# Optimization experiments

Hardware: AMD Instinct MI355X
Metric: run time of the kernel (lower is better)

Reference implementation:

```python
import jax, jax.numpy as jnp
import numpy as np

B, INPUT_DIM, EMB_DIM = 16384, 2048, 768
DOMAIN_NUM, MEMORY_NUM, TAU = 9, 10, 32.0


def setup_inputs() -> dict:
    key = jax.random.key(0)
    k1, k2, k3, k4, k5 = jax.random.split(key, 5)
    feature = jax.random.normal(k1, (B, INPUT_DIM), dtype=jnp.float32)
    category = jax.random.randint(k2, (B,), 0, DOMAIN_NUM, dtype=jnp.int64)
    # Linear(input_dim, emb_dim, bias=False) weights: [emb_dim, input_dim]
    W_topic = jax.random.normal(k3, (EMB_DIM, INPUT_DIM), dtype=jnp.float32) * 0.02
    W_domain = jax.random.normal(k4, (EMB_DIM, INPUT_DIM), dtype=jnp.float32) * 0.02
    # domain_num Embedding(memory_num, emb_dim) tables, stacked: [D, M, E]
    memory_tables = jax.random.normal(k5, (DOMAIN_NUM, MEMORY_NUM, EMB_DIM), dtype=jnp.float32)
    return {"feature": feature, "W_topic": W_topic, "W_domain": W_domain,
            "memory_tables": memory_tables, "category": category}


def reference(feature, W_topic, W_domain, memory_tables, category):
    eps = 1e-12
    # F.normalize(feature, p=2, dim=-1)
    norm = jnp.maximum(jnp.linalg.norm(feature, axis=-1, keepdims=True), eps)
    feat = feature / norm                                   # [B, I]
    # per-sample gather of each sample's category memory table: [B, M, E]
    mem = memory_tables[category]
    # faithful quirk: loop over domain_num indexes the BATCH dim of the stack
    D = memory_tables.shape[0]
    mems_d = mem[:D]                                        # [D, M, E]
    t = feat @ W_topic.T                                    # [B, E]
    topic_att = jax.nn.softmax(jnp.einsum('be,dme->bdm', t, mems_d) * TAU, axis=-1)
    sep = jnp.einsum('bdm,dme->bde', topic_att, mems_d)     # [B, D, E]
    dproj = feat @ W_domain.T                               # [B, E]
    domain_att = jax.nn.softmax(jnp.einsum('bde,be->bd', sep, dproj) * TAU, axis=-1)
    return domain_att[:, None, :]                           # [B, 1, D]
```

## Files before the change

kernel.cpp:

```cpp
#include <hip/hip_runtime.h>
#include <math.h>

#define TAU_F 32.0f

typedef __attribute__((ext_vector_type(8))) _Float16 half8;
typedef __attribute__((ext_vector_type(2))) __fp16 half2v;
typedef __attribute__((ext_vector_type(4))) float f32x4;

union HU { uint4 u; half8 v; };

__device__ __forceinline__ void sync_lds_only() {
    asm volatile("s_waitcnt lgkmcnt(0)" ::: "memory");
    __builtin_amdgcn_s_barrier();
}

__global__ __launch_bounds__(256) void gproj2(
    const float* __restrict__ Wt, const float* __restrict__ Wd,
    const float* __restrict__ mem, const int* __restrict__ cat,
    float* __restrict__ P)
{
    __shared__ float Ml[96 * 36];
    __shared__ float Wl[32 * 68];

    const int bid = blockIdx.x;
    const int mat = bid >> 7;
    const int ks  = (bid >> 5) & 3;
    const int ct  = bid & 31;
    const int c0  = ct * 64;
    const int tid = threadIdx.x;
    const float* __restrict__ W = mat ? Wd : Wt;

    const int tr = tid >> 4;
    const int tc = tid & 15;

    float acc[6][4];
    #pragma unroll
    for (int j = 0; j < 6; ++j)
        #pragma unroll
        for (int q = 0; q < 4; ++q) acc[j][q] = 0.f;

    for (int ch = 0; ch < 6; ++ch) {
        __syncthreads();
        #pragma unroll
        for (int p = 0; p < 3; ++p) {
            const int idx = tid + 256 * p;
            const int r   = idx >> 3;
            const int kq  = idx & 7;
            float4 v = make_float4(0.f, 0.f, 0.f, 0.f);
            if (r < 90) {
                const int d = r / 10;
                const int mrow = cat[d] * 10 + (r - d * 10);
                v = *(const float4*)(mem + (size_t)mrow * 768 + ks * 192 + ch * 32 + kq * 4);
            }
            *(float4*)(Ml + r * 36 + kq * 4) = v;
        }
        #pragma unroll
        for (int p = 0; p < 2; ++p) {
            const int idx = tid + 256 * p;
            const int e   = idx >> 4;
            const int c4  = (idx & 15) * 4;
            *(float4*)(Wl + e * 68 + c4) =
                *(const float4*)(W + (size_t)(ks * 192 + ch * 32 + e) * 2048 + c0 + c4);
        }
        __syncthreads();

        #pragma unroll
        for (int e = 0; e < 32; e += 4) {
            float4 m4[6], w4[4];
            #pragma unroll
            for (int j = 0; j < 6; ++j) m4[j] = *(const float4*)(Ml + (tr * 6 + j) * 36 + e);
            #pragma unroll
            for (int q = 0; q < 4; ++q) w4[q] = *(const float4*)(Wl + (e + q) * 68 + tc * 4);
            #pragma unroll
            for (int j = 0; j < 6; ++j) {
                const float mv[4] = {m4[j].x, m4[j].y, m4[j].z, m4[j].w};
                #pragma unroll
                for (int q = 0; q < 4; ++q) {
                    acc[j][0] = fmaf(mv[q], w4[q].x, acc[j][0]);
                    acc[j][1] = fmaf(mv[q], w4[q].y, acc[j][1]);
                    acc[j][2] = fmaf(mv[q], w4[q].z, acc[j][2]);
                    acc[j][3] = fmaf(mv[q], w4[q].w, acc[j][3]);
                }
            }
        }
    }

    #pragma unroll
    for (int j = 0; j < 6; ++j) {
        float4 v = make_float4(acc[j][0], acc[j][1], acc[j][2], acc[j][3]);
        *(float4*)(P + (size_t)ks * 393216 + (size_t)(mat * 96 + tr * 6 + j) * 2048 + c0 + tc * 4) = v;
    }
}

__global__ __launch_bounds__(256) void split_g3(
    const float* __restrict__ P, unsigned short* __restrict__ gB)
{
    const int u  = blockIdx.x * 256 + threadIdx.x;
    const int n  = u >> 8;
    const int k0 = (u & 255) * 8;

    float s[8] = {0.f, 0.f, 0.f, 0.f, 0.f, 0.f, 0.f, 0.f};
    #pragma unroll
    for (int ks = 0; ks < 4; ++ks) {
        const float4 a = *(const float4*)(P + (size_t)ks * 393216 + (size_t)n * 2048 + k0);
        const float4 b = *(const float4*)(P + (size_t)ks * 393216 + (size_t)n * 2048 + k0 + 4);
        s[0] += a.x; s[1] += a.y; s[2] += a.z; s[3] += a.w;
        s[4] += b.x; s[5] += b.y; s[6] += b.z; s[7] += b.w;
    }
    union { _Float16 h[8]; uint4 u4; } hi, lo;
    #pragma unroll
    for (int e = 0; e < 8; ++e) {
        const _Float16 h = (_Float16)s[e];
        hi.h[e] = h;
        lo.h[e] = (_Float16)(s[e] - (float)h);
    }
    const int kc = k0 >> 5;
    const int lq = (k0 >> 3) & 3;
    const int nq = n / 48;
    const int rm = n - nq * 48;
    const int j  = rm >> 4;
    const int lm = rm & 15;
    const size_t fH = (size_t)((kc * 12 + nq * 3 + j) * 2 + 0) * 512 + lq * 128 + lm * 8;
    const size_t fL = (size_t)((kc * 12 + nq * 3 + j) * 2 + 1) * 512 + lq * 128 + lm * 8;
    *(uint4*)(gB + fH) = hi.u4;
    *(uint4*)(gB + fL) = lo.u4;
}

__global__ __launch_bounds__(256, 2) void fused_ep(
    const float* __restrict__ feat, const unsigned short* __restrict__ gB,
    float* __restrict__ out)
{
    __shared__ __align__(16) unsigned char smraw[32 * 193 * 4];
    unsigned short* aS = (unsigned short*)smraw;
    float* sc = (float*)smraw;
    __shared__ float ssqS[32];

    const int tid  = threadIdx.x;
    const int row0 = blockIdx.x * 32;

    const int w  = tid >> 6, l = tid & 63;
    const int lm = l & 15,  lq = l >> 4;
    const int nq = (w + blockIdx.x) & 3;
    const bool topic = (nq < 2);
    const int sr = tid >> 3, kq = tid & 7;
    const int skf = kq >> 2, sk4 = kq & 3;

    f32x4 acc[2][3];
    #pragma unroll
    for (int i = 0; i < 2; ++i)
        #pragma unroll
        for (int j = 0; j < 3; ++j) acc[i][j] = (f32x4)0.f;
    float ssq = 0.f;

    const float* fbase = feat + (size_t)(row0 + sr) * 2048 + kq * 8;
    const unsigned short* bbase = gB + nq * 3072 + l * 8;

    auto cw = [&](int buf, float4 va, float4 vb) {
        const float xs[8] = {va.x, va.y, va.z, va.w, vb.x, vb.y, vb.z, vb.w};
        union { half2v h2[4]; uint4 u4; } uh, ul;
        #pragma unroll
        for (int e = 0; e < 4; ++e) {
            const float a = xs[2 * e], b = xs[2 * e + 1];
            ssq = fmaf(a, a, ssq); ssq = fmaf(b, b, ssq);
            half2v h = __builtin_amdgcn_cvt_pkrtz(a, b);
            uh.h2[e] = h;
            ul.h2[e] = __builtin_amdgcn_cvt_pkrtz(a - (float)h[0], b - (float)h[1]);
        }
        *(uint4*)(aS + (size_t)(((buf * 2 + 0) * 2 + skf) * 32 + sr) * 40 + sk4 * 8) = uh.u4;
        *(uint4*)(aS + (size_t)(((buf * 2 + 1) * 2 + skf) * 32 + sr) * 40 + sk4 * 8) = ul.u4;
    };

    float4 c0a = *(const float4*)(fbase);
    float4 c0b = *(const float4*)(fbase + 4);
    float4 c1a = *(const float4*)(fbase + 64);
    float4 c1b = *(const float4*)(fbase + 68);
    cw(0, c0a, c0b);
    sync_lds_only();

    for (int kt = 0; kt < 32; ++kt) {
        uint4 bh[6], bl[6];
        #pragma unroll
        for (int kf = 0; kf < 2; ++kf)
            #pragma unroll
            for (int j = 0; j < 3; ++j)
                bh[kf * 3 + j] = *(const uint4*)(bbase + (size_t)(2 * kt + kf) * 12288 + j * 1024);
        if (topic) {
            #pragma unroll
            for (int kf = 0; kf < 2; ++kf)
                #pragma unroll
                for (int j = 0; j < 3; ++j)
                    bl[kf * 3 + j] = *(const uint4*)(bbase + (size_t)(2 * kt + kf) * 12288 + j * 1024 + 512);
        }
        const int ka = (kt + 2 < 32) ? kt + 2 : 31;
        float4 cna = *(const float4*)(fbase + ka * 64);
        float4 cnb = *(const float4*)(fbase + ka * 64 + 4);

        if (kt < 31) cw((kt + 1) & 1, c1a, c1b);

        const int cb = kt & 1;
        half8 fh[2][2], fl[2][2];
        #pragma unroll
        for (int i = 0; i < 2; ++i)
            #pragma unroll
            for (int kf = 0; kf < 2; ++kf) {
                HU t;
                t.u = *(const uint4*)(aS + (size_t)(((cb * 2 + 0) * 2 + kf) * 32 + i * 16 + lm) * 40 + lq * 8);
                fh[i][kf] = t.v;
            }
        if (topic) {
            #pragma unroll
            for (int i = 0; i < 2; ++i)
                #pragma unroll
                for (int kf = 0; kf < 2; ++kf) {
                    HU t;
                    t.u = *(const uint4*)(aS + (size_t)(((cb * 2 + 1) * 2 + kf) * 32 + i * 16 + lm) * 40 + lq * 8);
                    fl[i][kf] = t.v;
                }
        }

        if (topic) {
            #pragma unroll
            for (int j = 0; j < 3; ++j)
                #pragma unroll
                for (int kf = 0; kf < 2; ++kf) {
                    HU h8, l8; h8.u = bh[kf * 3 + j]; l8.u = bl[kf * 3 + j];
                    #pragma unroll
                    for (int i = 0; i < 2; ++i) {
                        acc[i][j] = __builtin_amdgcn_mfma_f32_16x16x32_f16(fh[i][kf], h8.v, acc[i][j], 0, 0, 0);
                        acc[i][j] = __builtin_amdgcn_mfma_f32_16x16x32_f16(fh[i][kf], l8.v, acc[i][j], 0, 0, 0);
                        acc[i][j] = __builtin_amdgcn_mfma_f32_16x16x32_f16(fl[i][kf], h8.v, acc[i][j], 0, 0, 0);
                    }
                }
        } else {
            #pragma unroll
            for (int j = 0; j < 3; ++j)
                #pragma unroll
                for (int kf = 0; kf < 2; ++kf) {
                    HU h8; h8.u = bh[kf * 3 + j];
                    #pragma unroll
                    for (int i = 0; i < 2; ++i)
                        acc[i][j] = __builtin_amdgcn_mfma_f32_16x16x32_f16(fh[i][kf], h8.v, acc[i][j], 0, 0, 0);
                }
        }

        sync_lds_only();
        c1a = cna; c1b = cnb;
    }

    #pragma unroll
    for (int i = 0; i < 2; ++i)
        #pragma unroll
        for (int j = 0; j < 3; ++j)
            #pragma unroll
            for (int r4 = 0; r4 < 4; ++r4)
                sc[(i * 16 + lq * 4 + r4) * 193 + nq * 48 + j * 16 + lm] = acc[i][j][r4];

    ssq += __shfl_xor(ssq, 1, 64);
    ssq += __shfl_xor(ssq, 2, 64);
    ssq += __shfl_xor(ssq, 4, 64);
    if (kq == 0) ssqS[sr] = ssq;
    __syncthreads();

    if (tid < 64) {
        const int r  = tid >> 1, hf = tid & 1;
        const int nd = hf ? 4 : 5;
        const int d0 = hf ? 5 : 0;
        const float inv = TAU_F / fmaxf(sqrtf(ssqS[r]), 1e-12f);
        const float* scr = sc + (size_t)r * 193;
        float lg[5];
        float dmax = -1e30f;
        #pragma unroll
        for (int dd = 0; dd < 5; ++dd) {
            if (dd < nd) {
                const int d = d0 + dd;
                const float* v = scr + d * 10;
                const float* u = scr + 96 + d * 10;
                float mx = v[0];
                #pragma unroll
                for (int m = 1; m < 10; ++m) mx = fmaxf(mx, v[m]);
                float ssum = 0.f, dot = 0.f;
                #pragma unroll
                for (int m = 0; m < 10; ++m) {
                    const float p = __expf((v[m] - mx) * inv);
                    ssum += p;
                    dot = fmaf(p, u[m], dot);
                }
                const float lgt = (dot / ssum) * inv;
                lg[dd] = lgt;
                dmax = fmaxf(dmax, lgt);
            } else {
                lg[dd] = -1e30f;
            }
        }
        dmax = fmaxf(dmax, __shfl_xor(dmax, 1, 64));
        float s2 = 0.f;
        #pragma unroll
        for (int dd = 0; dd < 5; ++dd) {
            const float p = __expf(lg[dd] - dmax);
            lg[dd] = p;
            s2 += p;
        }
        s2 += __shfl_xor(s2, 1, 64);
        const float r2 = 1.0f / s2;
        #pragma unroll
        for (int dd = 0; dd < 5; ++dd)
            if (dd < nd)
                out[(size_t)(row0 + r) * 9 + d0 + dd] = lg[dd] * r2;
    }
}

extern "C" void kernel_launch(void* const* d_in, const int* in_sizes, int n_in,
                              void* d_out, int out_size, void* d_ws, size_t ws_size,
                              hipStream_t stream) {
    const float* feature = (const float*)d_in[0];
    const float* Wt      = (const float*)d_in[1];
    const float* Wd      = (const float*)d_in[2];
    const float* mem     = (const float*)d_in[3];
    const int*   cat     = (const int*)d_in[4];

    float* P  = (float*)d_ws;
    unsigned short* gB = (unsigned short*)((char*)d_ws + 50331648);
    float* out = (float*)d_out;

    gproj2<<<256, 256, 0, stream>>>(Wt, Wd, mem, cat, P);
    split_g3<<<192, 256, 0, stream>>>(P, gB);
    fused_ep<<<512, 256, 0, stream>>>(feature, gB, out);
}
```

Baseline: 243.0 us.

## Fuse weight-memory projection with fp16 hi/lo split, dropping K-split partials

The projection kernel no longer splits the 768-wide embedding reduction into four partial slabs. Each block now covers the full reduction for 16 output columns and writes the fp16 hi/lo split directly into the swizzled layout. This removes the separate reduce-and-split kernel, one launch, and the round trip of the fp32 partial buffer through global memory. In exchange each block runs a four-times-longer serial loop with less register reuse (one output column per thread) and issues scattered 2-byte stores.

```diff
diff --git a/kernel.cpp b/kernel.cpp
--- a/kernel.cpp
+++ b/kernel.cpp
@@ -14,116 +14,78 @@
     __builtin_amdgcn_s_barrier();
 }
 
-__global__ __launch_bounds__(256) void gproj2(
+__global__ __launch_bounds__(256) void gsplit(
     const float* __restrict__ Wt, const float* __restrict__ Wd,
     const float* __restrict__ mem, const int* __restrict__ cat,
-    float* __restrict__ P)
+    unsigned short* __restrict__ gB)
 {
-    __shared__ float Ml[96 * 36];
-    __shared__ float Wl[32 * 68];
+    __shared__ float Ml[96][36];
+    __shared__ float Wl[32][20];
 
     const int bid = blockIdx.x;
     const int mat = bid >> 7;
-    const int ks  = (bid >> 5) & 3;
-    const int ct  = bid & 31;
-    const int c0  = ct * 64;
+    const int c0  = (bid & 127) * 16;
     const int tid = threadIdx.x;
     const float* __restrict__ W = mat ? Wd : Wt;
 
     const int tr = tid >> 4;
     const int tc = tid & 15;
 
-    float acc[6][4];
-    #pragma unroll
-    for (int j = 0; j < 6; ++j)
-        #pragma unroll
-        for (int q = 0; q < 4; ++q) acc[j][q] = 0.f;
-
-    for (int ch = 0; ch < 6; ++ch) {
+    float acc[6] = {0.f, 0.f, 0.f, 0.f, 0.f, 0.f};
+
+    for (int ec = 0; ec < 24; ++ec) {
         __syncthreads();
         #pragma unroll
         for (int p = 0; p < 3; ++p) {
-            const int idx = tid + 256 * p;
-            const int r   = idx >> 3;
-            const int kq  = idx & 7;
+            const int u = tid + 256 * p;
+            const int r = u >> 3, q = u & 7;
             float4 v = make_float4(0.f, 0.f, 0.f, 0.f);
             if (r < 90) {
                 const int d = r / 10;
                 const int mrow = cat[d] * 10 + (r - d * 10);
-                v = *(const float4*)(mem + (size_t)mrow * 768 + ks * 192 + ch * 32 + kq * 4);
-            }
-            *(float4*)(Ml + r * 36 + kq * 4) = v;
-        }
-        #pragma unroll
-        for (int p = 0; p < 2; ++p) {
-            const int idx = tid + 256 * p;
-            const int e   = idx >> 4;
-            const int c4  = (idx & 15) * 4;
-            *(float4*)(Wl + e * 68 + c4) =
-                *(const float4*)(W + (size_t)(ks * 192 + ch * 32 + e) * 2048 + c0 + c4);
+                v = *(const float4*)(mem + (size_t)mrow * 768 + ec * 32 + q * 4);
+            }
+            *(float4*)(&Ml[r][q * 4]) = v;
+        }
+        if (tid < 128) {
+            const int e = tid >> 2, c4 = (tid & 3) * 4;
+            *(float4*)(&Wl[e][c4]) = *(const float4*)(W + (size_t)(ec * 32 + e) * 2048 + c0 + c4);
         }
         __syncthreads();
 
         #pragma unroll
         for (int e = 0; e < 32; e += 4) {
-            float4 m4[6], w4[4];
-            #pragma unroll
-            for (int j = 0; j < 6; ++j) m4[j] = *(const float4*)(Ml + (tr * 6 + j) * 36 + e);
-            #pragma unroll
-            for (int q = 0; q < 4; ++q) w4[q] = *(const float4*)(Wl + (e + q) * 68 + tc * 4);
+            float4 m4[6];
+            float w1[4];
+            #pragma unroll
+            for (int j = 0; j < 6; ++j) m4[j] = *(const float4*)(&Ml[tr * 6 + j][e]);
+            #pragma unroll
+            for (int q = 0; q < 4; ++q) w1[q] = Wl[e + q][tc];
             #pragma unroll
             for (int j = 0; j < 6; ++j) {
-                const float mv[4] = {m4[j].x, m4[j].y, m4[j].z, m4[j].w};
-                #pragma unroll
-                for (int q = 0; q < 4; ++q) {
-                    acc[j][0] = fmaf(mv[q], w4[q].x, acc[j][0]);
-                    acc[j][1] = fmaf(mv[q], w4[q].y, acc[j][1]);
-                    acc[j][2] = fmaf(mv[q], w4[q].z, acc[j][2]);
-                    acc[j][3] = fmaf(mv[q], w4[q].w, acc[j][3]);
-                }
-            }
-        }
-    }
-
+                acc[j] = fmaf(m4[j].x, w1[0], acc[j]);
+                acc[j] = fmaf(m4[j].y, w1[1], acc[j]);
+                acc[j] = fmaf(m4[j].z, w1[2], acc[j]);
+                acc[j] = fmaf(m4[j].w, w1[3], acc[j]);
+            }
+        }
+    }
+
+    const int k  = c0 + tc;
+    const int kc = k >> 5, lq = (k >> 3) & 3, km = k & 7;
     #pragma unroll
     for (int j = 0; j < 6; ++j) {
-        float4 v = make_float4(acc[j][0], acc[j][1], acc[j][2], acc[j][3]);
-        *(float4*)(P + (size_t)ks * 393216 + (size_t)(mat * 96 + tr * 6 + j) * 2048 + c0 + tc * 4) = v;
-    }
-}
-
-__global__ __launch_bounds__(256) void split_g3(
-    const float* __restrict__ P, unsigned short* __restrict__ gB)
-{
-    const int u  = blockIdx.x * 256 + threadIdx.x;
-    const int n  = u >> 8;
-    const int k0 = (u & 255) * 8;
-
-    float s[8] = {0.f, 0.f, 0.f, 0.f, 0.f, 0.f, 0.f, 0.f};
-    #pragma unroll
-    for (int ks = 0; ks < 4; ++ks) {
-        const float4 a = *(const float4*)(P + (size_t)ks * 393216 + (size_t)n * 2048 + k0);
-        const float4 b = *(const float4*)(P + (size_t)ks * 393216 + (size_t)n * 2048 + k0 + 4);
-        s[0] += a.x; s[1] += a.y; s[2] += a.z; s[3] += a.w;
-        s[4] += b.x; s[5] += b.y; s[6] += b.z; s[7] += b.w;
-    }
-    union { _Float16 h[8]; uint4 u4; } hi, lo;
-    #pragma unroll
-    for (int e = 0; e < 8; ++e) {
-        const _Float16 h = (_Float16)s[e];
-        hi.h[e] = h;
-        lo.h[e] = (_Float16)(s[e] - (float)h);
-    }
-    const int kc = k0 >> 5;
-    const int lq = (k0 >> 3) & 3;
-    const int nq = n / 48;
-    const int rm = n - nq * 48;
-    const int j  = rm >> 4;
-    const int lm = rm & 15;
-    const size_t fH = (size_t)((kc * 12 + nq * 3 + j) * 2 + 0) * 512 + lq * 128 + lm * 8;
-    const size_t fL = (size_t)((kc * 12 + nq * 3 + j) * 2 + 1) * 512 + lq * 128 + lm * 8;
-    *(uint4*)(gB + fH) = hi.u4;
-    *(uint4*)(gB + fL) = lo.u4;
+        const int n  = mat * 96 + tr * 6 + j;
+        const int nq = n / 48;
+        const int rm = n - nq * 48;
+        const int jj = rm >> 4, lm = rm & 15;
+        const size_t base = (size_t)(kc * 12 + nq * 3 + jj) * 1024 + lq * 128 + lm * 8 + km;
+        const float s = acc[j];
+        const _Float16 h = (_Float16)s;
+        const _Float16 l = (_Float16)(s - (float)h);
+        gB[base]       = *(const unsigned short*)&h;
+        gB[base + 512] = *(const unsigned short*)&l;
+    }
 }
 
 __global__ __launch_bounds__(256, 2) void fused_ep(
@@ -318,11 +280,9 @@
     const float* mem     = (const float*)d_in[3];
     const int*   cat     = (const int*)d_in[4];
 
-    float* P  = (float*)d_ws;
     unsigned short* gB = (unsigned short*)((char*)d_ws + 50331648);
     float* out = (float*)d_out;
 
-    gproj2<<<256, 256, 0, stream>>>(Wt, Wd, mem, cat, P);
-    split_g3<<<192, 256, 0, stream>>>(P, gB);
+    gsplit<<<256, 256, 0, stream>>>(Wt, Wd, mem, cat, gB);
     fused_ep<<<512, 256, 0, stream>>>(feature, gB, out);
 }
```

New measurement: 291.7 us. +20.0%, slower.
